# Optimization experiments

Measured on AMD Instinct MI355X. Metric: run time of the kernel, lower is better.

The kernel has to match this reference:

```python
import jax, jax.numpy as jnp
import numpy as np

B, S, I, H = 64, 512, 512, 1024


def setup_inputs() -> dict:
    key = jax.random.key(0)
    ks = jax.random.split(key, 14)
    bound = (1.0 / H) ** 0.5
    u = lambda k, shape: jax.random.uniform(k, shape, jnp.float32, -bound, bound)
    return {
        "inputs": jax.random.normal(ks[0], (B, S, I), jnp.float32),
        "hidden_states": jax.random.normal(ks[1], (1, B, H), jnp.float32),
        "w_ir": u(ks[2], (H, I)), "w_iz": u(ks[3], (H, I)), "w_in": u(ks[4], (H, I)),
        "b_ir": u(ks[5], (H,)), "b_iz": u(ks[6], (H,)), "b_in": u(ks[7], (H,)),
        "w_hr": u(ks[8], (H, H)), "w_hz": u(ks[9], (H, H)), "w_hn": u(ks[10], (H, H)),
        "b_hr": u(ks[11], (H,)), "b_hz": u(ks[12], (H,)), "b_hn": u(ks[13], (H,)),
    }


def gru_forward(inputs, hidden_states, w_ir, w_iz, w_in, b_ir, b_iz, b_in,
                w_hr, w_hz, w_hn, b_hr, b_hz, b_hn):
    h0 = hidden_states[0]  # (B, H)
    # Original loop starts at t=1, so inputs[:, 0] is unused.
    x = inputs[:, 1:]  # (B, S-1, I)
    # Precompute all input projections (cuDNN-style), then scan the recurrence.
    xr = jnp.einsum('bsi,hi->sbh', x, w_ir) + b_ir
    xz = jnp.einsum('bsi,hi->sbh', x, w_iz) + b_iz
    xn = jnp.einsum('bsi,hi->sbh', x, w_in) + b_in

    def step(h, xs):
        xr_t, xz_t, xn_t = xs
        r = jax.nn.sigmoid(xr_t + h @ w_hr.T + b_hr)
        n = jnp.tanh(xn_t + r * (h @ w_hn.T + b_hn))
        z = jax.nn.sigmoid(xz_t + h @ w_hz.T + b_hz)
        h = (1.0 - z) * n + z * h
        return h, h

    h_last, hs = jax.lax.scan(step, h0, (xr, xz, xn))  # hs: (S-1, B, H)
    outputs = jnp.concatenate([h0[None], hs], axis=0).swapaxes(0, 1)  # (B, S, H)
    return outputs, h_last[None]  # final hidden keeps leading dim 1


def reference(inputs, hidden_states, w_ir, w_iz, w_in, b_ir, b_iz, b_in,
              w_hr, w_hz, w_hn, b_hr, b_hz, b_hn):
    return gru_forward(inputs, hidden_states, w_ir, w_iz, w_in, b_ir, b_iz, b_in,
                       w_hr, w_hz, w_hn, b_hr, b_hz, b_hn)
```

## Files before the change

kernel.cpp:

```cpp
#include <hip/hip_runtime.h>
#include <hip/hip_bf16.h>

typedef __bf16 bf16x8 __attribute__((ext_vector_type(8)));
typedef float  f32x4  __attribute__((ext_vector_type(4)));

#define Bq 64
#define Sq 512
#define Iq 512
#define Hq 1024
#define TSTEPS 511
#define MB 16
#define NCOLS 32
#define SHq (Sq*Hq)

__device__ inline unsigned short f2bf(float f){ return __builtin_bit_cast(unsigned short, (__bf16)f); }
__device__ inline float bf2f(unsigned short u){ return (float)__builtin_bit_cast(__bf16, u); }

__device__ inline unsigned ah_addr(unsigned row, unsigned k){ return ((row<<11) + (k<<1)) ^ ((row&7)<<4); }
__device__ inline unsigned ax_addr(unsigned row, unsigned k){ return ((row<<10) + (k<<1)) ^ ((row&7)<<4); }

__device__ inline bf16x8 load_wfrag(const float* p){
  float4 a = *(const float4*)p;
  float4 b = *(const float4*)(p+4);
  bf16x8 w;
  w[0]=(__bf16)a.x; w[1]=(__bf16)a.y; w[2]=(__bf16)a.z; w[3]=(__bf16)a.w;
  w[4]=(__bf16)b.x; w[5]=(__bf16)b.y; w[6]=(__bf16)b.z; w[7]=(__bf16)b.w;
  return w;
}

__global__ __launch_bounds__(512, 2) void gru_kernel(
    const float* __restrict__ x, const float* __restrict__ h0,
    const float* __restrict__ w_ir, const float* __restrict__ w_iz, const float* __restrict__ w_in_,
    const float* __restrict__ b_ir, const float* __restrict__ b_iz, const float* __restrict__ b_in_,
    const float* __restrict__ w_hr, const float* __restrict__ w_hz, const float* __restrict__ w_hn,
    const float* __restrict__ b_hr, const float* __restrict__ b_hz, const float* __restrict__ b_hn,
    float* __restrict__ out, void* ws)
{
  __shared__ unsigned short Ah[MB*Hq];
  __shared__ unsigned short Ax[MB*Iq];
  __shared__ float P[2*4*4*256];
  __shared__ float biasR[NCOLS], biasZ[NCOLS], biasNX[NCOLS], biasNH[NCOLS];

  const unsigned tid    = threadIdx.x;
  const unsigned bid    = blockIdx.x;
  const unsigned g      = bid & 3;
  const unsigned colblk = bid >> 2;
  const unsigned colbase= colblk * NCOLS;
  const unsigned lane   = tid & 63;
  const unsigned wave   = tid >> 6;
  const unsigned ct     = wave >> 2;
  const unsigned q      = wave & 3;
  const unsigned l15    = lane & 15;
  const unsigned l4     = lane >> 4;

  unsigned* flags = (unsigned*)ws + (size_t)g*64;
  unsigned short* hb0 = (unsigned short*)((char*)ws + 1024);
  unsigned short* hb1 = hb0 + Bq*Hq;

  if (tid < NCOLS) {
    unsigned c = colbase + tid;
    biasR[tid]  = b_ir[c] + b_hr[c];
    biasZ[tid]  = b_iz[c] + b_hz[c];
    biasNX[tid] = b_in_[c];
    biasNH[tid] = b_hn[c];
  }

  if (tid < 256) {
    unsigned row = tid >> 4, cp = (tid & 15) << 1;
    unsigned b = g*MB + row;
    unsigned hcol = colbase + cp;
    float2 v = *(const float2*)(h0 + (size_t)b*Hq + hcol);
    *(float2*)(out + (size_t)b*SHq + hcol) = v;
    unsigned pv = (unsigned)f2bf(v.x) | ((unsigned)f2bf(v.y) << 16);
    __hip_atomic_store((unsigned*)(hb0 + (size_t)b*Hq + hcol), pv,
                       __ATOMIC_RELAXED, __HIP_MEMORY_SCOPE_AGENT);
  }
  __syncthreads();
  if (tid == 0)
    __hip_atomic_store(flags + colblk, 1u, __ATOMIC_RELAXED, __HIP_MEMORY_SCOPE_AGENT);

  const unsigned hcf = colbase + ct*16 + l15;
  bf16x8 wRX[4], wZX[4], wNX[4];
  bf16x8 wRH[8], wZH[8], wNH[8];
  #pragma unroll
  for (int j = 0; j < 4; ++j) {
    unsigned ks = q*4 + j;
    wRX[j] = load_wfrag(w_ir  + (size_t)hcf*Iq + ks*32 + l4*8);
    wZX[j] = load_wfrag(w_iz  + (size_t)hcf*Iq + ks*32 + l4*8);
    wNX[j] = load_wfrag(w_in_ + (size_t)hcf*Iq + ks*32 + l4*8);
  }
  #pragma unroll
  for (int j = 0; j < 8; ++j) {
    unsigned ks = q*8 + j;
    wRH[j] = load_wfrag(w_hr + (size_t)hcf*Hq + ks*32 + l4*8);
    wZH[j] = load_wfrag(w_hz + (size_t)hcf*Hq + ks*32 + l4*8);
    wNH[j] = load_wfrag(w_hn + (size_t)hcf*Hq + ks*32 + l4*8);
  }

  const unsigned srow = tid >> 5, sli = tid & 31;

  unsigned cur = 0;
  for (int t = 0; t < TSTEPS; ++t) {
    const unsigned short* hs = cur ? hb1 : hb0;
    unsigned short*       hd = cur ? hb0 : hb1;

    {
      const float* xs = x + ((size_t)(g*MB+srow)*Sq + (size_t)(t+1))*Iq;
      #pragma unroll
      for (int i = 0; i < 4; ++i) {
        unsigned e0 = (sli + 32*i) * 4;
        float4 v = *(const float4*)(xs + e0);
        unsigned long long pv = (unsigned long long)f2bf(v.x)
                              | ((unsigned long long)f2bf(v.y) << 16)
                              | ((unsigned long long)f2bf(v.z) << 32)
                              | ((unsigned long long)f2bf(v.w) << 48);
        *(unsigned long long*)((char*)Ax + ax_addr(srow, e0)) = pv;
      }
    }

    if (tid < 32) {
      unsigned tgt = (unsigned)t + 1;
      for (;;) {
        unsigned v = __hip_atomic_load(flags + tid, __ATOMIC_RELAXED, __HIP_MEMORY_SCOPE_AGENT);
        if (__all((int)(v >= tgt))) break;
      }
    }
    __syncthreads();

    unsigned long long hv[8];
    {
      const unsigned long long* srcs = (const unsigned long long*)(hs + (size_t)(g*MB+srow)*Hq);
      #pragma unroll
      for (int i = 0; i < 8; ++i)
        hv[i] = __hip_atomic_load(srcs + sli + 32*i, __ATOMIC_RELAXED, __HIP_MEMORY_SCOPE_AGENT);
    }

    f32x4 accR={0.f,0.f,0.f,0.f}, accZ={0.f,0.f,0.f,0.f}, accNX={0.f,0.f,0.f,0.f}, accNH={0.f,0.f,0.f,0.f};
    #pragma unroll
    for (int j = 0; j < 4; ++j) {
      unsigned ks = q*4 + j;
      bf16x8 a = *(const bf16x8*)((char*)Ax + ax_addr(l15, ks*32 + l4*8));
      accR  = __builtin_amdgcn_mfma_f32_16x16x32_bf16(a, wRX[j], accR, 0, 0, 0);
      accZ  = __builtin_amdgcn_mfma_f32_16x16x32_bf16(a, wZX[j], accZ, 0, 0, 0);
      accNX = __builtin_amdgcn_mfma_f32_16x16x32_bf16(a, wNX[j], accNX, 0, 0, 0);
    }

    #pragma unroll
    for (int i = 0; i < 8; ++i)
      *(unsigned long long*)((char*)Ah + ah_addr(srow, (sli + 32*i)*4)) = hv[i];
    __syncthreads();

    #pragma unroll
    for (int j = 0; j < 8; ++j) {
      unsigned ks = q*8 + j;
      bf16x8 a = *(const bf16x8*)((char*)Ah + ah_addr(l15, ks*32 + l4*8));
      accR  = __builtin_amdgcn_mfma_f32_16x16x32_bf16(a, wRH[j], accR, 0, 0, 0);
      accZ  = __builtin_amdgcn_mfma_f32_16x16x32_bf16(a, wZH[j], accZ, 0, 0, 0);
      accNH = __builtin_amdgcn_mfma_f32_16x16x32_bf16(a, wNH[j], accNH, 0, 0, 0);
    }

    {
      float* base = P + (ct*16 + q)*256;
      #pragma unroll
      for (int i = 0; i < 4; ++i) {
        unsigned e = (l4*4 + i)*16 + l15;
        base[0    + e] = accR[i];
        base[1024 + e] = accZ[i];
        base[2048 + e] = accNX[i];
        base[3072 + e] = accNH[i];
      }
    }
    __syncthreads();

    if (tid < 256) {
      const unsigned ctl = tid >> 7, idx = tid & 127;
      const unsigned row = idx >> 3, cp = (idx & 7) << 1;
      const unsigned b = g*MB + row;
      float hn2[2];
      #pragma unroll
      for (int cc = 0; cc < 2; ++cc) {
        unsigned col = cp + cc;
        unsigned e = row*16 + col;
        float pr = 0.f, pz = 0.f, pnx = 0.f, pnh = 0.f;
        #pragma unroll
        for (int qq = 0; qq < 4; ++qq) {
          const float* pbase = P + (ctl*16 + qq)*256 + e;
          pr  += pbase[0];
          pz  += pbase[1024];
          pnx += pbase[2048];
          pnh += pbase[3072];
        }
        unsigned lc = ctl*16 + col;
        float r = 1.f/(1.f + __expf(-(pr + biasR[lc])));
        float z = 1.f/(1.f + __expf(-(pz + biasZ[lc])));
        float nin = pnx + biasNX[lc] + r*(pnh + biasNH[lc]);
        float e2 = __expf(2.f*nin);
        float n = 1.f - 2.f/(e2 + 1.f);
        unsigned hcol = colbase + lc;
        float hold = bf2f(*(const unsigned short*)((char*)Ah + ah_addr(row, hcol)));
        hn2[cc] = (1.f - z)*n + z*hold;
      }
      unsigned hcol0 = colbase + ctl*16 + cp;
      *(float2*)(out + (size_t)b*SHq + (size_t)(t+1)*Hq + hcol0) = make_float2(hn2[0], hn2[1]);
      if (t == TSTEPS-1)
        *(float2*)(out + (size_t)Bq*SHq + (size_t)b*Hq + hcol0) = make_float2(hn2[0], hn2[1]);
      unsigned pv = (unsigned)f2bf(hn2[0]) | ((unsigned)f2bf(hn2[1]) << 16);
      __hip_atomic_store((unsigned*)(hd + (size_t)b*Hq + hcol0), pv,
                         __ATOMIC_RELAXED, __HIP_MEMORY_SCOPE_AGENT);
    }
    __syncthreads();
    if (tid == 0 && t < TSTEPS-1)
      __hip_atomic_store(flags + colblk, (unsigned)t + 2, __ATOMIC_RELAXED, __HIP_MEMORY_SCOPE_AGENT);

    cur ^= 1;
  }
}

extern "C" void kernel_launch(void* const* d_in, const int* in_sizes, int n_in,
                              void* d_out, int out_size, void* d_ws, size_t ws_size,
                              hipStream_t stream) {
  const float* x     = (const float*)d_in[0];
  const float* h0    = (const float*)d_in[1];
  const float* w_ir  = (const float*)d_in[2];
  const float* w_iz  = (const float*)d_in[3];
  const float* w_in_ = (const float*)d_in[4];
  const float* b_ir  = (const float*)d_in[5];
  const float* b_iz  = (const float*)d_in[6];
  const float* b_in_ = (const float*)d_in[7];
  const float* w_hr  = (const float*)d_in[8];
  const float* w_hz  = (const float*)d_in[9];
  const float* w_hn  = (const float*)d_in[10];
  const float* b_hr  = (const float*)d_in[11];
  const float* b_hz  = (const float*)d_in[12];
  const float* b_hn  = (const float*)d_in[13];
  float* out = (float*)d_out;

  hipMemsetAsync(d_ws, 0, 1024, stream);

  void* args[] = { (void*)&x, (void*)&h0, (void*)&w_ir, (void*)&w_iz, (void*)&w_in_,
                   (void*)&b_ir, (void*)&b_iz, (void*)&b_in_, (void*)&w_hr, (void*)&w_hz,
                   (void*)&w_hn, (void*)&b_hr, (void*)&b_hz, (void*)&b_hn,
                   (void*)&out, (void*)&d_ws };
  hipLaunchCooperativeKernel((void*)gru_kernel, dim3(128), dim3(512), args, 0, stream);
}
```

Baseline: 1.497 ms.

## Replace per-block flag barrier with tagged hidden-state data polling and prefetch inputs

Drops the per-step flag array and instead embeds a parity tag in the low mantissa bit of each bf16 hidden value, so consumers poll the data itself until every element carries the expected tag. This removes the flag store/poll round trip and one block-wide barrier per step. The epilogue now uses all 512 threads with one column each, and the next timestep's inputs are prefetched into registers. Stealing the low bit slightly perturbs the bf16 hidden state, and the workspace memset grows to cover the double buffers.

```diff
diff --git a/kernel.cpp b/kernel.cpp
--- a/kernel.cpp
+++ b/kernel.cpp
@@ -12,6 +12,7 @@
 #define MB 16
 #define NCOLS 32
 #define SHq (Sq*Hq)
+#define TAGM 0x0001000100010001ull
 
 __device__ inline unsigned short f2bf(float f){ return __builtin_bit_cast(unsigned short, (__bf16)f); }
 __device__ inline float bf2f(unsigned short u){ return (float)__builtin_bit_cast(__bf16, u); }
@@ -28,7 +29,7 @@
   return w;
 }
 
-__global__ __launch_bounds__(512, 2) void gru_kernel(
+__global__ __launch_bounds__(512, 1) void gru_kernel(
     const float* __restrict__ x, const float* __restrict__ h0,
     const float* __restrict__ w_ir, const float* __restrict__ w_iz, const float* __restrict__ w_in_,
     const float* __restrict__ b_ir, const float* __restrict__ b_iz, const float* __restrict__ b_in_,
@@ -52,9 +53,9 @@
   const unsigned q      = wave & 3;
   const unsigned l15    = lane & 15;
   const unsigned l4     = lane >> 4;
-
-  unsigned* flags = (unsigned*)ws + (size_t)g*64;
-  unsigned short* hb0 = (unsigned short*)((char*)ws + 1024);
+  const unsigned srow   = tid >> 5, sli = tid & 31;
+
+  unsigned short* hb0 = (unsigned short*)ws;
   unsigned short* hb1 = hb0 + Bq*Hq;
 
   if (tid < NCOLS) {
@@ -65,19 +66,14 @@
     biasNH[tid] = b_hn[c];
   }
 
-  if (tid < 256) {
-    unsigned row = tid >> 4, cp = (tid & 15) << 1;
-    unsigned b = g*MB + row;
-    unsigned hcol = colbase + cp;
-    float2 v = *(const float2*)(h0 + (size_t)b*Hq + hcol);
-    *(float2*)(out + (size_t)b*SHq + hcol) = v;
-    unsigned pv = (unsigned)f2bf(v.x) | ((unsigned)f2bf(v.y) << 16);
-    __hip_atomic_store((unsigned*)(hb0 + (size_t)b*Hq + hcol), pv,
+  {
+    unsigned b = g*MB + srow, hcol = colbase + sli;
+    float v = h0[(size_t)b*Hq + hcol];
+    out[(size_t)b*SHq + hcol] = v;
+    unsigned short u = (unsigned short)(f2bf(v) & ~1u);
+    __hip_atomic_store(hb0 + (size_t)b*Hq + hcol, u,
                        __ATOMIC_RELAXED, __HIP_MEMORY_SCOPE_AGENT);
   }
-  __syncthreads();
-  if (tid == 0)
-    __hip_atomic_store(flags + colblk, 1u, __ATOMIC_RELAXED, __HIP_MEMORY_SCOPE_AGENT);
 
   const unsigned hcf = colbase + ct*16 + l15;
   bf16x8 wRX[4], wZX[4], wNX[4];
@@ -97,43 +93,58 @@
     wNH[j] = load_wfrag(w_hn + (size_t)hcf*Hq + ks*32 + l4*8);
   }
 
-  const unsigned srow = tid >> 5, sli = tid & 31;
-
-  unsigned cur = 0;
+  float4 xpf[4];
+  {
+    const float* xs = x + ((size_t)(g*MB+srow)*Sq + 1)*Iq;
+    #pragma unroll
+    for (int i = 0; i < 4; ++i) xpf[i] = *(const float4*)(xs + (sli + 32*i)*4);
+  }
+
   for (int t = 0; t < TSTEPS; ++t) {
-    const unsigned short* hs = cur ? hb1 : hb0;
-    unsigned short*       hd = cur ? hb0 : hb1;
+    const unsigned short* hs = (t & 1) ? hb1 : hb0;
+    unsigned short*       hd = (t & 1) ? hb0 : hb1;
+    const unsigned long long want = ((t >> 1) & 1) ? TAGM : 0ull;
+    const unsigned tagd = ((t + 1) >> 1) & 1;
+
+    #pragma unroll
+    for (int i = 0; i < 4; ++i) {
+      float4 v = xpf[i];
+      unsigned long long pv = (unsigned long long)f2bf(v.x)
+                            | ((unsigned long long)f2bf(v.y) << 16)
+                            | ((unsigned long long)f2bf(v.z) << 32)
+                            | ((unsigned long long)f2bf(v.w) << 48);
+      *(unsigned long long*)((char*)Ax + ax_addr(srow, (sli + 32*i)*4)) = pv;
+    }
+
+    unsigned long long hv[8];
+    const unsigned long long* srcs = (const unsigned long long*)(hs + (size_t)(g*MB+srow)*Hq);
+    #pragma unroll
+    for (int i = 0; i < 8; ++i)
+      hv[i] = __hip_atomic_load(srcs + sli + 32*i, __ATOMIC_RELAXED, __HIP_MEMORY_SCOPE_AGENT);
+    for (;;) {
+      unsigned stale = 0;
+      #pragma unroll
+      for (int i = 0; i < 8; ++i)
+        if ((hv[i] & TAGM) != want) stale |= 1u << i;
+      if (!stale) break;
+      __builtin_amdgcn_s_sleep(1);
+      #pragma unroll
+      for (int i = 0; i < 8; ++i)
+        if (stale & (1u << i))
+          hv[i] = __hip_atomic_load(srcs + sli + 32*i, __ATOMIC_RELAXED, __HIP_MEMORY_SCOPE_AGENT);
+    }
 
     {
-      const float* xs = x + ((size_t)(g*MB+srow)*Sq + (size_t)(t+1))*Iq;
-      #pragma unroll
-      for (int i = 0; i < 4; ++i) {
-        unsigned e0 = (sli + 32*i) * 4;
-        float4 v = *(const float4*)(xs + e0);
-        unsigned long long pv = (unsigned long long)f2bf(v.x)
-                              | ((unsigned long long)f2bf(v.y) << 16)
-                              | ((unsigned long long)f2bf(v.z) << 32)
-                              | ((unsigned long long)f2bf(v.w) << 48);
-        *(unsigned long long*)((char*)Ax + ax_addr(srow, e0)) = pv;
-      }
-    }
-
-    if (tid < 32) {
-      unsigned tgt = (unsigned)t + 1;
-      for (;;) {
-        unsigned v = __hip_atomic_load(flags + tid, __ATOMIC_RELAXED, __HIP_MEMORY_SCOPE_AGENT);
-        if (__all((int)(v >= tgt))) break;
-      }
-    }
+      int tt = (t + 2 <= 511) ? (t + 2) : 511;
+      const float* xs = x + ((size_t)(g*MB+srow)*Sq + (size_t)tt)*Iq;
+      #pragma unroll
+      for (int i = 0; i < 4; ++i) xpf[i] = *(const float4*)(xs + (sli + 32*i)*4);
+    }
+
+    #pragma unroll
+    for (int i = 0; i < 8; ++i)
+      *(unsigned long long*)((char*)Ah + ah_addr(srow, (sli + 32*i)*4)) = hv[i];
     __syncthreads();
-
-    unsigned long long hv[8];
-    {
-      const unsigned long long* srcs = (const unsigned long long*)(hs + (size_t)(g*MB+srow)*Hq);
-      #pragma unroll
-      for (int i = 0; i < 8; ++i)
-        hv[i] = __hip_atomic_load(srcs + sli + 32*i, __ATOMIC_RELAXED, __HIP_MEMORY_SCOPE_AGENT);
-    }
 
     f32x4 accR={0.f,0.f,0.f,0.f}, accZ={0.f,0.f,0.f,0.f}, accNX={0.f,0.f,0.f,0.f}, accNH={0.f,0.f,0.f,0.f};
     #pragma unroll
@@ -144,12 +155,6 @@
       accZ  = __builtin_amdgcn_mfma_f32_16x16x32_bf16(a, wZX[j], accZ, 0, 0, 0);
       accNX = __builtin_amdgcn_mfma_f32_16x16x32_bf16(a, wNX[j], accNX, 0, 0, 0);
     }
-
-    #pragma unroll
-    for (int i = 0; i < 8; ++i)
-      *(unsigned long long*)((char*)Ah + ah_addr(srow, (sli + 32*i)*4)) = hv[i];
-    __syncthreads();
-
     #pragma unroll
     for (int j = 0; j < 8; ++j) {
       unsigned ks = q*8 + j;
@@ -158,6 +163,10 @@
       accZ  = __builtin_amdgcn_mfma_f32_16x16x32_bf16(a, wZH[j], accZ, 0, 0, 0);
       accNH = __builtin_amdgcn_mfma_f32_16x16x32_bf16(a, wNH[j], accNH, 0, 0, 0);
     }
+
+    const unsigned rrow = srow, lc = sli;
+    const unsigned hcol = colbase + lc;
+    float hold = bf2f(*(const unsigned short*)((char*)Ah + ah_addr(rrow, hcol)));
 
     {
       float* base = P + (ct*16 + q)*256;
@@ -172,47 +181,33 @@
     }
     __syncthreads();
 
-    if (tid < 256) {
-      const unsigned ctl = tid >> 7, idx = tid & 127;
-      const unsigned row = idx >> 3, cp = (idx & 7) << 1;
-      const unsigned b = g*MB + row;
-      float hn2[2];
-      #pragma unroll
-      for (int cc = 0; cc < 2; ++cc) {
-        unsigned col = cp + cc;
-        unsigned e = row*16 + col;
-        float pr = 0.f, pz = 0.f, pnx = 0.f, pnh = 0.f;
-        #pragma unroll
-        for (int qq = 0; qq < 4; ++qq) {
-          const float* pbase = P + (ctl*16 + qq)*256 + e;
-          pr  += pbase[0];
-          pz  += pbase[1024];
-          pnx += pbase[2048];
-          pnh += pbase[3072];
-        }
-        unsigned lc = ctl*16 + col;
-        float r = 1.f/(1.f + __expf(-(pr + biasR[lc])));
-        float z = 1.f/(1.f + __expf(-(pz + biasZ[lc])));
-        float nin = pnx + biasNX[lc] + r*(pnh + biasNH[lc]);
-        float e2 = __expf(2.f*nin);
-        float n = 1.f - 2.f/(e2 + 1.f);
-        unsigned hcol = colbase + lc;
-        float hold = bf2f(*(const unsigned short*)((char*)Ah + ah_addr(row, hcol)));
-        hn2[cc] = (1.f - z)*n + z*hold;
+    {
+      const unsigned ctl = lc >> 4, col = lc & 15;
+      const unsigned b = g*MB + rrow;
+      const unsigned e = rrow*16 + col;
+      float pr = 0.f, pz = 0.f, pnx = 0.f, pnh = 0.f;
+      #pragma unroll
+      for (int qq = 0; qq < 4; ++qq) {
+        const float* pbase = P + (ctl*16 + qq)*256 + e;
+        pr  += pbase[0];
+        pz  += pbase[1024];
+        pnx += pbase[2048];
+        pnh += pbase[3072];
       }
-      unsigned hcol0 = colbase + ctl*16 + cp;
-      *(float2*)(out + (size_t)b*SHq + (size_t)(t+1)*Hq + hcol0) = make_float2(hn2[0], hn2[1]);
+      float r = 1.f/(1.f + __expf(-(pr + biasR[lc])));
+      float z = 1.f/(1.f + __expf(-(pz + biasZ[lc])));
+      float nin = pnx + biasNX[lc] + r*(pnh + biasNH[lc]);
+      float e2 = __expf(2.f*nin);
+      float n = 1.f - 2.f/(e2 + 1.f);
+      float hn = (1.f - z)*n + z*hold;
+
+      unsigned short u = (unsigned short)((f2bf(hn) & ~1u) | tagd);
+      __hip_atomic_store(hd + (size_t)b*Hq + hcol, u,
+                         __ATOMIC_RELAXED, __HIP_MEMORY_SCOPE_AGENT);
+      out[(size_t)b*SHq + (size_t)(t+1)*Hq + hcol] = hn;
       if (t == TSTEPS-1)
-        *(float2*)(out + (size_t)Bq*SHq + (size_t)b*Hq + hcol0) = make_float2(hn2[0], hn2[1]);
-      unsigned pv = (unsigned)f2bf(hn2[0]) | ((unsigned)f2bf(hn2[1]) << 16);
-      __hip_atomic_store((unsigned*)(hd + (size_t)b*Hq + hcol0), pv,
-                         __ATOMIC_RELAXED, __HIP_MEMORY_SCOPE_AGENT);
-    }
-    __syncthreads();
-    if (tid == 0 && t < TSTEPS-1)
-      __hip_atomic_store(flags + colblk, (unsigned)t + 2, __ATOMIC_RELAXED, __HIP_MEMORY_SCOPE_AGENT);
-
-    cur ^= 1;
+        out[(size_t)Bq*SHq + (size_t)b*Hq + hcol] = hn;
+    }
   }
 }
 
@@ -235,7 +230,7 @@
   const float* b_hn  = (const float*)d_in[13];
   float* out = (float*)d_out;
 
-  hipMemsetAsync(d_ws, 0, 1024, stream);
+  hipMemsetAsync(d_ws, 0xFF, (size_t)2 * Bq * Hq * sizeof(unsigned short), stream);
 
   void* args[] = { (void*)&x, (void*)&h0, (void*)&w_ir, (void*)&w_iz, (void*)&w_in_,
                    (void*)&b_ir, (void*)&b_iz, (void*)&b_in_, (void*)&w_hr, (void*)&w_hz,
```

Result: faster. 1.325 ms (-11.5%).
